# Performance work log

Measured on AMD Instinct MI355X. Metric: run time of the kernel, lower is better.

The kernel has to match this reference:

```python
import jax, jax.numpy as jnp
import numpy as np

TEMPERATURE = 0.05
K = 5
EPS = 1e-8
B, D = 4096, 512


def setup_inputs() -> dict:
    key = jax.random.key(0)
    k1, k2 = jax.random.split(key)
    f1 = jax.random.normal(k1, (B, D), dtype=jnp.float32)
    f2 = jax.random.normal(k2, (B, D), dtype=jnp.float32)
    # contrastive embeddings are typically L2-normalized; also keeps exp(dot/T) finite in fp32
    f1 = f1 / jnp.linalg.norm(f1, axis=-1, keepdims=True)
    f2 = f2 / jnp.linalg.norm(f2, axis=-1, keepdims=True)
    return {"features_1": f1, "features_2": f2}


def reference(features_1, features_2):
    b = features_1.shape[0]
    n = 2 * b
    feats = jnp.concatenate([features_1, features_2], axis=0)  # [2B, D]
    # cosine similarity via normalize + single GEMM (avoids O(N^2*D) broadcast)
    norms = jnp.linalg.norm(feats, axis=-1, keepdims=True)
    fn = feats / jnp.maximum(norms, EPS)
    sim = fn @ fn.T  # [2B, 2B]
    # k+1 nearest (self is the top-1 on the diagonal), drop first column
    _, nbr_idx = jax.lax.top_k(sim, K + 1)
    nbr_idx = nbr_idx[:, 1:]  # [2B, K]
    # positive pair term uses raw dot product (not cosine), as in the source
    pos = jnp.exp(jnp.sum(features_1 * features_2, axis=-1) / TEMPERATURE)  # [B]
    pos = jnp.concatenate([pos, pos], axis=0)  # [2B]
    neg = jnp.exp(sim / TEMPERATURE)  # [2B, 2B]
    diag = jnp.arange(n)
    neg = neg.at[diag, diag].set(0.0)  # mask self-similarity
    rows = diag[:, None]  # [2B, 1]
    neg = neg.at[rows, nbr_idx].set(0.0)  # zero out k nearest neighbors
    ng = jnp.sum(neg, axis=-1)  # [2B]
    loss = jnp.mean(-jnp.log(pos / (ng + pos)))
    return loss
```

## Files before the change

kernel.cpp:

```cpp
#include <hip/hip_runtime.h>
#include <hip/hip_bf16.h>

#define B_ROWS 4096
#define D_DIM  512
#define N_ROWS 8192
#define EPS_N  1e-8f
#define INV_T  20.0f
#define FACT   0.0281778328298626f
#define CSPLIT 8
#define BM 256
#define BN 256
#define COLS_PER_CHUNK (N_ROWS / CSPLIT)
#define STRIPS (COLS_PER_CHUNK / BN)
#define NIT (STRIPS * 4)
#define TILE_BYTES 16384
#define BUF_BYTES  32768
#define PANEL_BYTES 65536
#define KITER_BYTES 16384

typedef __attribute__((ext_vector_type(16))) float floatx16;
typedef __attribute__((ext_vector_type(8)))  int   intx8;
typedef __attribute__((ext_vector_type(4)))  int   intx4;

#define AS1C(p) ((const __attribute__((address_space(1))) void*)(p))
#define AS3(p)  ((__attribute__((address_space(3))) void*)(p))

#define SC1 0x7F7F7F7F
#define MXMFMA4(A, B, C) \
  __builtin_amdgcn_mfma_scale_f32_32x32x64_f8f6f4((A), (B), (C), 4, 4, 0, SC1, 0, SC1)

__device__ __forceinline__ intx4 ldsFrag16(const char* base, int row, int kg) {
  return *(const intx4*)(base + kg * 4096 + row * 16);
}

__device__ __forceinline__ void insert5(float (&t)[5], float v) {
  float n0 = fmaxf(t[0], v);
  float n1 = __builtin_amdgcn_fmed3f(v, t[1], t[0]);
  float n2 = __builtin_amdgcn_fmed3f(v, t[2], t[1]);
  float n3 = __builtin_amdgcn_fmed3f(v, t[3], t[2]);
  float n4 = __builtin_amdgcn_fmed3f(v, t[4], t[3]);
  t[0] = n0; t[1] = n1; t[2] = n2; t[3] = n3; t[4] = n4;
}

__device__ __forceinline__ void scan_acc(floatx16 (&acc)[2][2], float (&sum)[2],
                                         float (&top)[2][5]) {
  #pragma unroll
  for (int rb = 0; rb < 2; ++rb)
    #pragma unroll
    for (int cb = 0; cb < 2; ++cb)
      #pragma unroll
      for (int r = 0; r < 16; ++r) {
        float ev = exp2f(acc[rb][cb][r] * FACT);
        sum[rb] += ev;
        insert5(top[rb], ev);
      }
}

__device__ __forceinline__ unsigned enc_fp4(float y) {
  float f = fminf(fabsf(y), 6.0f);
  float c1 = rintf(f + f);
  float c2 = rintf(f - 2.0f) + 4.0f;
  float c3 = rintf((f - 4.0f) * 0.5f) + 6.0f;
  float c = (f < 2.0f) ? c1 : ((f < 4.0f) ? c2 : c3);
  return (unsigned)c | ((__float_as_uint(y) >> 31) << 3);
}

__device__ __forceinline__ void stage_tile(const char* gA_t, const char* gB_t,
                                           char* buf, int wave, int lane) {
  const char* src = ((wave < 8) ? gA_t : gB_t) + (wave & 7) * 2048 + lane * 16;
  char* dst = buf + ((wave < 8) ? 0 : TILE_BYTES) + (wave & 7) * 2048;
  #pragma unroll
  for (int q = 0; q < 2; ++q)
    __builtin_amdgcn_global_load_lds(AS1C(src + q * 1024), AS3(dst + q * 1024), 16, 0, 0);
}

__global__ __launch_bounds__(256) void prep_kernel(
    const float* __restrict__ f1, const float* __restrict__ f2,
    unsigned char* __restrict__ fnb4, float* __restrict__ dots)
{
  int row = blockIdx.x;
  int t = threadIdx.x;
  const float* r1 = f1 + (size_t)row * D_DIM;
  const float* r2 = f2 + (size_t)row * D_DIM;
  float2 a = *(const float2*)(r1 + 2 * t);
  float2 b = *(const float2*)(r2 + 2 * t);
  float s1 = a.x * a.x + a.y * a.y;
  float s2 = b.x * b.x + b.y * b.y;
  float d  = a.x * b.x + a.y * b.y;
  #pragma unroll
  for (int off = 32; off >= 1; off >>= 1) {
    s1 += __shfl_down(s1, off);
    s2 += __shfl_down(s2, off);
    d  += __shfl_down(d, off);
  }
  __shared__ float red[4][3];
  __shared__ float bc[2];
  int wave = t >> 6, lane = t & 63;
  if (lane == 0) { red[wave][0] = s1; red[wave][1] = s2; red[wave][2] = d; }
  __syncthreads();
  if (t == 0) {
    float S1 = red[0][0] + red[1][0] + red[2][0] + red[3][0];
    float S2 = red[0][1] + red[1][1] + red[2][1] + red[3][1];
    float Dd = red[0][2] + red[1][2] + red[2][2] + red[3][2];
    bc[0] = 1.0f / fmaxf(sqrtf(S1), EPS_N);
    bc[1] = 1.0f / fmaxf(sqrtf(S2), EPS_N);
    dots[row] = Dd;
  }
  __syncthreads();
  if (t < 128) {
    int q = t & 63;
    int is2 = t >> 6;
    const float* src = (is2 ? f2 : f1) + (size_t)row * D_DIM + q * 8;
    float sc = bc[is2] * 32.0f;
    float4 v0 = *(const float4*)(src);
    float4 v1 = *(const float4*)(src + 4);
    unsigned p = enc_fp4(v0.x * sc);
    p |= enc_fp4(v0.y * sc) << 4;
    p |= enc_fp4(v0.z * sc) << 8;
    p |= enc_fp4(v0.w * sc) << 12;
    p |= enc_fp4(v1.x * sc) << 16;
    p |= enc_fp4(v1.y * sc) << 20;
    p |= enc_fp4(v1.z * sc) << 24;
    p |= enc_fp4(v1.w * sc) << 28;
    int grow = row + is2 * B_ROWS;
    int panel = grow >> 8, rin = grow & 255;
    int kg = q >> 2;
    *(unsigned*)(fnb4 + (size_t)panel * PANEL_BYTES + kg * 4096 + rin * 16
                 + (q & 3) * 4) = p;
  }
}

__global__ __launch_bounds__(1024, 4) void sim_kernel(
    const unsigned char* __restrict__ fnb4,
    float* __restrict__ partials)
{
  __shared__ int4 lds4[4096];
  char* lds = (char*)lds4;

  int bx = blockIdx.x;
  int xcd = bx & 7, kk = bx >> 3;
  int rt = xcd * 4 + (kk & 3);
  int chunk = kk >> 2;
  int rowbase = rt * BM;
  int chunkbase = chunk * COLS_PER_CHUNK;

  int t = threadIdx.x;
  int wave = t >> 6, lane = t & 63;
  int wr = wave >> 2, wc = wave & 3;
  int l31 = lane & 31, lh = lane >> 5;

  float sum[2];
  float top[2][5];
  floatx16 acc[2][2];
  #pragma unroll
  for (int rb = 0; rb < 2; ++rb) {
    sum[rb] = 0.f;
    #pragma unroll
    for (int k = 0; k < 5; ++k) top[rb][k] = 0.f;
    #pragma unroll
    for (int cb = 0; cb < 2; ++cb)
      #pragma unroll
      for (int e = 0; e < 16; ++e) acc[rb][cb][e] = 0.0f;
  }

  const char* gA  = (const char*)fnb4 + (size_t)rt * PANEL_BYTES;
  const char* gB0 = (const char*)fnb4 + (size_t)(chunk * 4) * PANEL_BYTES;

  stage_tile(gA, gB0, lds, wave, lane);
  __syncthreads();

  intx4 z4 = {0, 0, 0, 0};
  for (int it = 0; it < NIT; ++it) {
    int strip = it >> 2, kstep = it & 3, cur = it & 1;

    if (it + 1 < NIT) {
      int ns = (it + 1) >> 2, nk = (it + 1) & 3;
      stage_tile(gA + nk * KITER_BYTES,
                 gB0 + (size_t)ns * PANEL_BYTES + nk * KITER_BYTES,
                 lds + (cur ^ 1) * BUF_BYTES, wave, lane);
    }

    const char* As = lds + cur * BUF_BYTES;
    const char* Bs = As + TILE_BYTES;
    __builtin_amdgcn_s_setprio(1);
    #pragma unroll
    for (int m = 0; m < 2; ++m) {
      int kg = m * 2 + lh;
      intx4 rf0 = ldsFrag16(As, wr * 64 + l31,      kg);
      intx4 rf1 = ldsFrag16(As, wr * 64 + 32 + l31, kg);
      intx4 cf0 = ldsFrag16(Bs, wc * 64 + l31,      kg);
      intx4 cf1 = ldsFrag16(Bs, wc * 64 + 32 + l31, kg);
      intx8 R0 = __builtin_shufflevector(rf0, z4, 0, 1, 2, 3, 4, 5, 6, 7);
      intx8 R1 = __builtin_shufflevector(rf1, z4, 0, 1, 2, 3, 4, 5, 6, 7);
      intx8 C0 = __builtin_shufflevector(cf0, z4, 0, 1, 2, 3, 4, 5, 6, 7);
      intx8 C1 = __builtin_shufflevector(cf1, z4, 0, 1, 2, 3, 4, 5, 6, 7);
      acc[0][0] = MXMFMA4(C0, R0, acc[0][0]);
      acc[0][1] = MXMFMA4(C1, R0, acc[0][1]);
      acc[1][0] = MXMFMA4(C0, R1, acc[1][0]);
      acc[1][1] = MXMFMA4(C1, R1, acc[1][1]);
    }
    __builtin_amdgcn_s_setprio(0);

    if (kstep == 3) {
      bool dwave = (rowbase + wr * 64) == (chunkbase + strip * BN + wc * 64);
      if (dwave && (((l31 >> 2) & 1) == lh)) {
        int rd = (l31 & 3) | (((l31 >> 3) & 3) << 2);
        acc[0][0][rd] = -1e30f;
        acc[1][1][rd] = -1e30f;
      }
      scan_acc(acc, sum, top);
      #pragma unroll
      for (int rb = 0; rb < 2; ++rb)
        #pragma unroll
        for (int cb = 0; cb < 2; ++cb)
          #pragma unroll
          for (int e = 0; e < 16; ++e) acc[rb][cb][e] = 0.0f;
    }

    __syncthreads();
  }

  #pragma unroll
  for (int rb = 0; rb < 2; ++rb) {
    sum[rb] += __shfl_xor(sum[rb], 32);
    float pt[5];
    #pragma unroll
    for (int k = 0; k < 5; ++k) pt[k] = __shfl_xor(top[rb][k], 32);
    #pragma unroll
    for (int k = 0; k < 5; ++k) insert5(top[rb], pt[k]);
  }

  float* mbuf = (float*)lds;
  if (lane < 32) {
    #pragma unroll
    for (int rb = 0; rb < 2; ++rb) {
      float* dst = mbuf + (size_t)(((wave * 2 + rb) * 32) + lane) * 6;
      dst[0] = sum[rb];
      #pragma unroll
      for (int k = 0; k < 5; ++k) dst[1 + k] = top[rb][k];
    }
  }
  __syncthreads();
  if (t < 256) {
    int wr2 = t >> 6, rb2 = (t >> 5) & 1, r31 = t & 31;
    float s = 0.0f;
    float a5[5] = {0.f, 0.f, 0.f, 0.f, 0.f};
    #pragma unroll
    for (int wc2 = 0; wc2 < 4; ++wc2) {
      int w = wr2 * 4 + wc2;
      const float* src = mbuf + (size_t)(((w * 2 + rb2) * 32) + r31) * 6;
      s += src[0];
      #pragma unroll
      for (int k = 0; k < 5; ++k) insert5(a5, src[1 + k]);
    }
    int grow = rowbase + t;
    float* dst = partials + ((size_t)grow * CSPLIT + chunk) * 6;
    dst[0] = s;
    #pragma unroll
    for (int k = 0; k < 5; ++k) dst[1 + k] = a5[k];
  }
}

__global__ __launch_bounds__(256) void finalize1_kernel(
    const float* __restrict__ partials, const float* __restrict__ dots,
    float* __restrict__ bpart)
{
  int row = blockIdx.x * 256 + threadIdx.x;
  const float* p = partials + (size_t)row * (CSPLIT * 6);
  float s = 0.0f;
  float a5[5] = {0.f, 0.f, 0.f, 0.f, 0.f};
  #pragma unroll
  for (int c = 0; c < CSPLIT; ++c) {
    s += p[c * 6];
    #pragma unroll
    for (int k = 0; k < 5; ++k) insert5(a5, p[c * 6 + 1 + k]);
  }
  float ng = s - (a5[0] + a5[1] + a5[2] + a5[3] + a5[4]);
  float dv = dots[row & (B_ROWS - 1)];
  float acc = __logf(ng + __expf(dv * INV_T)) - dv * INV_T;

  #pragma unroll
  for (int off = 32; off >= 1; off >>= 1) acc += __shfl_down(acc, off);
  __shared__ float red[4];
  int wave = threadIdx.x >> 6, lane = threadIdx.x & 63;
  if (lane == 0) red[wave] = acc;
  __syncthreads();
  if (threadIdx.x == 0)
    bpart[blockIdx.x] = red[0] + red[1] + red[2] + red[3];
}

__global__ __launch_bounds__(64) void finalize2_kernel(
    const float* __restrict__ bpart, float* __restrict__ out)
{
  int t = threadIdx.x;
  float v = (t < 32) ? bpart[t] : 0.0f;
  #pragma unroll
  for (int off = 32; off >= 1; off >>= 1) v += __shfl_down(v, off);
  if (t == 0) out[0] = v / (float)N_ROWS;
}

extern "C" void kernel_launch(void* const* d_in, const int* in_sizes, int n_in,
                              void* d_out, int out_size, void* d_ws, size_t ws_size,
                              hipStream_t stream) {
  const float* f1 = (const float*)d_in[0];
  const float* f2 = (const float*)d_in[1];
  float* out = (float*)d_out;
  char* ws = (char*)d_ws;

  unsigned char* fnb4 = (unsigned char*)ws;
  float* dots = (float*)(ws + (size_t)4 * 1024 * 1024);
  float* partials = (float*)(ws + (size_t)4 * 1024 * 1024 + 65536);
  float* bpart = (float*)(ws + (size_t)8 * 1024 * 1024);

  prep_kernel<<<B_ROWS, 256, 0, stream>>>(f1, f2, fnb4, dots);
  sim_kernel<<<(N_ROWS / BM) * CSPLIT, 1024, 0, stream>>>(fnb4, partials);
  finalize1_kernel<<<32, 256, 0, stream>>>(partials, dots, bpart);
  finalize2_kernel<<<1, 64, 0, stream>>>(bpart, out);
}
```

Measured before the change: 59.80 us.

## Keep full A panel resident in LDS and overlap softmax scan with next strip MFMAs

Loads the whole 256-row A panel into LDS once and streams only narrower 128-column B strips, double-buffered, so each barrier covers a full K loop rather than a quarter. Accumulators are ping-ponged so the exp/top-5 scan of the previous strip interleaves with MFMAs of the current strip. Top-5 tracking moves to raw dot values, with exp applied only to the final five, and the sum is split into two partial sums to shorten the dependency chain. LDS use doubles to 128 KB, which may reduce occupancy per CU.

```diff
diff --git a/kernel.cpp b/kernel.cpp
--- a/kernel.cpp
+++ b/kernel.cpp
@@ -9,14 +9,12 @@
 #define FACT   0.0281778328298626f
 #define CSPLIT 8
 #define BM 256
-#define BN 256
+#define BN 128
 #define COLS_PER_CHUNK (N_ROWS / CSPLIT)
 #define STRIPS (COLS_PER_CHUNK / BN)
-#define NIT (STRIPS * 4)
-#define TILE_BYTES 16384
-#define BUF_BYTES  32768
+#define A_BYTES 65536
+#define B_BYTES 32768
 #define PANEL_BYTES 65536
-#define KITER_BYTES 16384
 
 typedef __attribute__((ext_vector_type(16))) float floatx16;
 typedef __attribute__((ext_vector_type(8)))  int   intx8;
@@ -24,14 +22,11 @@
 
 #define AS1C(p) ((const __attribute__((address_space(1))) void*)(p))
 #define AS3(p)  ((__attribute__((address_space(3))) void*)(p))
+#define W8(a) __builtin_shufflevector((a), (a), 0, 1, 2, 3, -1, -1, -1, -1)
 
 #define SC1 0x7F7F7F7F
 #define MXMFMA4(A, B, C) \
   __builtin_amdgcn_mfma_scale_f32_32x32x64_f8f6f4((A), (B), (C), 4, 4, 0, SC1, 0, SC1)
-
-__device__ __forceinline__ intx4 ldsFrag16(const char* base, int row, int kg) {
-  return *(const intx4*)(base + kg * 4096 + row * 16);
-}
 
 __device__ __forceinline__ void insert5(float (&t)[5], float v) {
   float n0 = fmaxf(t[0], v);
@@ -42,20 +37,6 @@
   t[0] = n0; t[1] = n1; t[2] = n2; t[3] = n3; t[4] = n4;
 }
 
-__device__ __forceinline__ void scan_acc(floatx16 (&acc)[2][2], float (&sum)[2],
-                                         float (&top)[2][5]) {
-  #pragma unroll
-  for (int rb = 0; rb < 2; ++rb)
-    #pragma unroll
-    for (int cb = 0; cb < 2; ++cb)
-      #pragma unroll
-      for (int r = 0; r < 16; ++r) {
-        float ev = exp2f(acc[rb][cb][r] * FACT);
-        sum[rb] += ev;
-        insert5(top[rb], ev);
-      }
-}
-
 __device__ __forceinline__ unsigned enc_fp4(float y) {
   float f = fminf(fabsf(y), 6.0f);
   float c1 = rintf(f + f);
@@ -63,15 +44,6 @@
   float c3 = rintf((f - 4.0f) * 0.5f) + 6.0f;
   float c = (f < 2.0f) ? c1 : ((f < 4.0f) ? c2 : c3);
   return (unsigned)c | ((__float_as_uint(y) >> 31) << 3);
-}
-
-__device__ __forceinline__ void stage_tile(const char* gA_t, const char* gB_t,
-                                           char* buf, int wave, int lane) {
-  const char* src = ((wave < 8) ? gA_t : gB_t) + (wave & 7) * 2048 + lane * 16;
-  char* dst = buf + ((wave < 8) ? 0 : TILE_BYTES) + (wave & 7) * 2048;
-  #pragma unroll
-  for (int q = 0; q < 2; ++q)
-    __builtin_amdgcn_global_load_lds(AS1C(src + q * 1024), AS3(dst + q * 1024), 16, 0, 0);
 }
 
 __global__ __launch_bounds__(256) void prep_kernel(
@@ -134,7 +106,7 @@
     const unsigned char* __restrict__ fnb4,
     float* __restrict__ partials)
 {
-  __shared__ int4 lds4[4096];
+  __shared__ int4 lds4[8192];
   char* lds = (char*)lds4;
 
   int bx = blockIdx.x;
@@ -149,80 +121,92 @@
   int wr = wave >> 2, wc = wave & 3;
   int l31 = lane & 31, lh = lane >> 5;
 
-  float sum[2];
-  float top[2][5];
-  floatx16 acc[2][2];
-  #pragma unroll
-  for (int rb = 0; rb < 2; ++rb) {
-    sum[rb] = 0.f;
-    #pragma unroll
-    for (int k = 0; k < 5; ++k) top[rb][k] = 0.f;
-    #pragma unroll
-    for (int cb = 0; cb < 2; ++cb)
-      #pragma unroll
-      for (int e = 0; e < 16; ++e) acc[rb][cb][e] = 0.0f;
-  }
+  int arow16 = (wr * 64 + l31) * 16;
+  int bcol16 = (wc * 32 + l31) * 16;
 
   const char* gA  = (const char*)fnb4 + (size_t)rt * PANEL_BYTES;
   const char* gB0 = (const char*)fnb4 + (size_t)(chunk * 4) * PANEL_BYTES;
 
-  stage_tile(gA, gB0, lds, wave, lane);
-  __syncthreads();
-
-  intx4 z4 = {0, 0, 0, 0};
-  for (int it = 0; it < NIT; ++it) {
-    int strip = it >> 2, kstep = it & 3, cur = it & 1;
-
-    if (it + 1 < NIT) {
-      int ns = (it + 1) >> 2, nk = (it + 1) & 3;
-      stage_tile(gA + nk * KITER_BYTES,
-                 gB0 + (size_t)ns * PANEL_BYTES + nk * KITER_BYTES,
-                 lds + (cur ^ 1) * BUF_BYTES, wave, lane);
-    }
-
-    const char* As = lds + cur * BUF_BYTES;
-    const char* Bs = As + TILE_BYTES;
-    __builtin_amdgcn_s_setprio(1);
-    #pragma unroll
-    for (int m = 0; m < 2; ++m) {
-      int kg = m * 2 + lh;
-      intx4 rf0 = ldsFrag16(As, wr * 64 + l31,      kg);
-      intx4 rf1 = ldsFrag16(As, wr * 64 + 32 + l31, kg);
-      intx4 cf0 = ldsFrag16(Bs, wc * 64 + l31,      kg);
-      intx4 cf1 = ldsFrag16(Bs, wc * 64 + 32 + l31, kg);
-      intx8 R0 = __builtin_shufflevector(rf0, z4, 0, 1, 2, 3, 4, 5, 6, 7);
-      intx8 R1 = __builtin_shufflevector(rf1, z4, 0, 1, 2, 3, 4, 5, 6, 7);
-      intx8 C0 = __builtin_shufflevector(cf0, z4, 0, 1, 2, 3, 4, 5, 6, 7);
-      intx8 C1 = __builtin_shufflevector(cf1, z4, 0, 1, 2, 3, 4, 5, 6, 7);
-      acc[0][0] = MXMFMA4(C0, R0, acc[0][0]);
-      acc[0][1] = MXMFMA4(C1, R0, acc[0][1]);
-      acc[1][0] = MXMFMA4(C0, R1, acc[1][0]);
-      acc[1][1] = MXMFMA4(C1, R1, acc[1][1]);
-    }
-    __builtin_amdgcn_s_setprio(0);
-
-    if (kstep == 3) {
-      bool dwave = (rowbase + wr * 64) == (chunkbase + strip * BN + wc * 64);
-      if (dwave && (((l31 >> 2) & 1) == lh)) {
-        int rd = (l31 & 3) | (((l31 >> 3) & 3) << 2);
-        acc[0][0][rd] = -1e30f;
-        acc[1][1][rd] = -1e30f;
+  float sum[2][2];
+  float top[2][5];
+  floatx16 accA[2], accB[2];
+  #pragma unroll
+  for (int rb = 0; rb < 2; ++rb) {
+    sum[rb][0] = sum[rb][1] = 0.f;
+    #pragma unroll
+    for (int k = 0; k < 5; ++k) top[rb][k] = -3.0e38f;
+    #pragma unroll
+    for (int e = 0; e < 16; ++e) { accA[rb][e] = 0.0f; accB[rb][e] = 0.0f; }
+  }
+
+  {
+    const char* sa = gA + wave * 4096 + lane * 16;
+    char* da = lds + wave * 4096;
+    #pragma unroll
+    for (int q = 0; q < 4; ++q)
+      __builtin_amdgcn_global_load_lds(AS1C(sa + q * 1024), AS3(da + q * 1024), 16, 0, 0);
+    const char* sb = gB0 + wave * 4096 + lane * 16;
+    char* db = lds + A_BYTES + wave * 2048;
+    #pragma unroll
+    for (int q = 0; q < 2; ++q)
+      __builtin_amdgcn_global_load_lds(AS1C(sb + q * 1024), AS3(db + q * 1024), 16, 0, 0);
+  }
+  __syncthreads();
+
+  auto scanP = [&](floatx16 (&acc)[2], int sp) {
+    int d = (chunkbase + sp * BN + wc * 32) - (rowbase + wr * 64);
+    if ((d == 0 || d == 32) && lh == ((l31 >> 2) & 1)) {
+      int rd = (l31 & 3) | (((l31 >> 3) & 3) << 2);
+      acc[d >> 5][rd] = -1e30f;
+    }
+    #pragma unroll
+    for (int rb = 0; rb < 2; ++rb)
+      #pragma unroll
+      for (int r = 0; r < 16; ++r) {
+        float v = acc[rb][r];
+        sum[rb][r & 1] += exp2f(v * FACT);
+        insert5(top[rb], v);
+        acc[rb][r] = 0.0f;
       }
-      scan_acc(acc, sum, top);
+  };
+
+  auto iter = [&](int s, floatx16 (&accC)[2], floatx16 (&accP)[2], bool doScan) {
+    const char* Bs = lds + A_BYTES + (s & 1) * B_BYTES;
+    if (s + 1 < STRIPS) {
+      const char* sb = gB0 + (size_t)((s + 1) >> 1) * PANEL_BYTES
+                     + wave * 4096 + ((s + 1) & 1) * 2048 + lane * 16;
+      char* db = lds + A_BYTES + ((s + 1) & 1) * B_BYTES + wave * 2048;
       #pragma unroll
-      for (int rb = 0; rb < 2; ++rb)
-        #pragma unroll
-        for (int cb = 0; cb < 2; ++cb)
-          #pragma unroll
-          for (int e = 0; e < 16; ++e) acc[rb][cb][e] = 0.0f;
-    }
-
+      for (int q = 0; q < 2; ++q)
+        __builtin_amdgcn_global_load_lds(AS1C(sb + q * 1024), AS3(db + q * 1024), 16, 0, 0);
+    }
+    if (doScan) scanP(accP, s - 1);
+    #pragma unroll
+    for (int kq = 0; kq < 8; ++kq) {
+      int kg = kq * 2 + lh;
+      intx4 rf0 = *(const intx4*)(lds + kg * 4096 + arow16);
+      intx4 rf1 = *(const intx4*)(lds + kg * 4096 + arow16 + 512);
+      intx4 cf  = *(const intx4*)(Bs  + kg * 2048 + bcol16);
+      accC[0] = MXMFMA4(W8(cf), W8(rf0), accC[0]);
+      accC[1] = MXMFMA4(W8(cf), W8(rf1), accC[1]);
+    }
     __syncthreads();
-  }
-
+  };
+
+  iter(0, accA, accB, false);
+  #pragma unroll 1
+  for (int ss = 0; ss < 3; ++ss) {
+    iter(2 * ss + 1, accB, accA, true);
+    iter(2 * ss + 2, accA, accB, true);
+  }
+  iter(7, accB, accA, true);
+  scanP(accB, 7);
+
+  float rsum[2];
   #pragma unroll
   for (int rb = 0; rb < 2; ++rb) {
-    sum[rb] += __shfl_xor(sum[rb], 32);
+    rsum[rb] = sum[rb][0] + sum[rb][1];
+    rsum[rb] += __shfl_xor(rsum[rb], 32);
     float pt[5];
     #pragma unroll
     for (int k = 0; k < 5; ++k) pt[k] = __shfl_xor(top[rb][k], 32);
@@ -235,7 +219,7 @@
     #pragma unroll
     for (int rb = 0; rb < 2; ++rb) {
       float* dst = mbuf + (size_t)(((wave * 2 + rb) * 32) + lane) * 6;
-      dst[0] = sum[rb];
+      dst[0] = rsum[rb];
       #pragma unroll
       for (int k = 0; k < 5; ++k) dst[1 + k] = top[rb][k];
     }
@@ -244,7 +228,7 @@
   if (t < 256) {
     int wr2 = t >> 6, rb2 = (t >> 5) & 1, r31 = t & 31;
     float s = 0.0f;
-    float a5[5] = {0.f, 0.f, 0.f, 0.f, 0.f};
+    float a5[5] = {-3.0e38f, -3.0e38f, -3.0e38f, -3.0e38f, -3.0e38f};
     #pragma unroll
     for (int wc2 = 0; wc2 < 4; ++wc2) {
       int w = wr2 * 4 + wc2;
@@ -257,7 +241,7 @@
     float* dst = partials + ((size_t)grow * CSPLIT + chunk) * 6;
     dst[0] = s;
     #pragma unroll
-    for (int k = 0; k < 5; ++k) dst[1 + k] = a5[k];
+    for (int k = 0; k < 5; ++k) dst[1 + k] = exp2f(a5[k] * FACT);
   }
 }
 
```

New measurement: 95.55 us (median of 3 runs). 1.6x slower.
